# Performance work log

Hardware: AMD Instinct MI355X
Metric: run time of the kernel (lower is better)

The kernel has to match this reference:

```python
import jax, jax.numpy as jnp
import numpy as np

NX = 96
N_NODES = 6 * NX * NX          # 55296 cubed-sphere grid points
N_EDGES = 4 * N_NODES          # ~4-neighbor connectivity
HID = 32
NUM_STEPS = 3


def setup_inputs() -> dict:
    key = jax.random.key(0)
    ks = jax.random.split(key, 12)
    s = 0.05
    inp = {
        "in_node_features": jax.random.normal(ks[0], (2, 6, NX, NX, 32), jnp.float32),
        "edge_relation": jax.random.normal(ks[1], (N_EDGES, 4), jnp.float32),
        "pw1": jax.random.normal(ks[2], (32, HID), jnp.float32) * s,
        "pb1": jnp.zeros((HID,), jnp.float32),
        "pw2": jax.random.normal(ks[3], (HID, HID), jnp.float32) * s,
        "pb2": jnp.zeros((HID,), jnp.float32),
        "ew1": jax.random.normal(ks[4], (4, 32), jnp.float32) * s,
        "eb1": jnp.zeros((32,), jnp.float32),
        "ew2": jax.random.normal(ks[5], (32, HID * HID), jnp.float32) * s,
        "eb2": jnp.zeros((HID * HID,), jnp.float32),
        "conv_b": jnp.zeros((HID,), jnp.float32),
        "gru_w_ih": jax.random.normal(ks[6], (3 * HID, HID), jnp.float32) * s,
        "gru_w_hh": jax.random.normal(ks[7], (3 * HID, HID), jnp.float32) * s,
        "gru_b_ih": jnp.zeros((3 * HID,), jnp.float32),
        "gru_b_hh": jnp.zeros((3 * HID,), jnp.float32),
        "edge_src": jax.random.randint(ks[8], (N_EDGES,), 0, N_NODES, jnp.int32),
        "edge_dst": jax.random.randint(ks[9], (N_EDGES,), 0, N_NODES, jnp.int32),
    }
    return inp


def reference(in_node_features, edge_relation, pw1, pb1, pw2, pb2,
              ew1, eb1, ew2, eb2, conv_b,
              gru_w_ih, gru_w_hh, gru_b_ih, gru_b_hh,
              edge_src, edge_dst):
    B, T, nx1, nx2, C = in_node_features.shape
    N = T * nx1 * nx2
    H = pw2.shape[1]

    x = in_node_features.reshape(B, N, C)
    # project_node_features: Linear -> ReLU -> Linear
    h0 = jnp.maximum(x @ pw1 + pb1, 0.0) @ pw2 + pb2          # [B, N, H]

    # edge network (same every step): Linear -> ReLU -> Linear -> [E, H, H]
    We = (jnp.maximum(edge_relation @ ew1 + eb1, 0.0) @ ew2 + eb2)
    We = We.reshape(-1, H, H)                                  # [E, H, H]

    def seg_sum(m):  # m: [E, H] -> [N, H]
        return jax.ops.segment_sum(m, edge_dst, num_segments=N)

    def step(carry, _):
        node, hidden = carry                                   # each [B, N, H]
        # NNConv: gather src feats, per-edge matmul, scatter-sum to dst
        msg = jnp.einsum('beh,eho->beo', node[:, edge_src], We)  # [B, E, H]
        agg = jax.vmap(seg_sum)(msg) + conv_b                    # [B, N, H]
        node = jnp.maximum(agg, 0.0)                             # ReLU
        # single GRU step (seq_len = 1)
        gx = node @ gru_w_ih.T + gru_b_ih                        # [B, N, 3H]
        gh = hidden @ gru_w_hh.T + gru_b_hh
        r = jax.nn.sigmoid(gx[..., :H] + gh[..., :H])
        z = jax.nn.sigmoid(gx[..., H:2 * H] + gh[..., H:2 * H])
        n = jnp.tanh(gx[..., 2 * H:] + r * gh[..., 2 * H:])
        hidden = (1.0 - z) * n + z * hidden
        return (hidden, hidden), None

    (node, _), _ = jax.lax.scan(step, (h0, h0), None, length=NUM_STEPS)
    return node.reshape(B, T, nx1, nx2, H)
```

## Files before the change

kernel.cpp:

```cpp
#include <hip/hip_runtime.h>

typedef unsigned short u16;
typedef short s16x8 __attribute__((ext_vector_type(8)));
typedef float f32x4 __attribute__((ext_vector_type(4)));
typedef float f32x2 __attribute__((ext_vector_type(2)));

#define NNODES 55296
#define NEDGES 221184
#define ROWS   110592

__device__ __forceinline__ u16 f2bf(float f) {
    union { float f; unsigned u; } v; v.f = f;
    unsigned r = (v.u + 0x7fffu + ((v.u >> 16) & 1u)) >> 16;
    return (u16)r;
}
__device__ __forceinline__ float bf2f(u16 u) {
    return __uint_as_float(((unsigned)u) << 16);
}

__global__ __launch_bounds__(256) void pack_bfrag(
    const float* __restrict__ src, u16* __restrict__ dst_hi, u16* __restrict__ dst_lo,
    int ntiles, int ncols, int trans)
{
    int idx = blockIdx.x * 256 + threadIdx.x;
    if (idx >= ntiles * 512) return;
    int t = idx >> 9, rr = idx & 511, lane = rr >> 3, j = rr & 7;
    int k = (lane >> 4) * 8 + j;
    int n = t * 16 + (lane & 15);
    float v = trans ? src[n * 32 + k] : src[k * ncols + n];
    u16 hb = f2bf(v);
    dst_hi[idx] = hb;
    if (dst_lo) dst_lo[idx] = f2bf(v - bf2f(hb));
}

__global__ __launch_bounds__(256) void edgemlp_kernel(
    const float* __restrict__ er, const float* __restrict__ ew1,
    const float* __restrict__ eb1, u16* __restrict__ rbf)
{
    __shared__ float er_lds[32];
    __shared__ float w_lds[128];
    __shared__ float b_lds[32];
    int tid = threadIdx.x;
    int e8 = blockIdx.x * 8;
    if (tid < 32) er_lds[tid] = er[e8 * 4 + tid];
    else if (tid < 160) w_lds[tid - 32] = ew1[tid - 32];
    else if (tid < 192) b_lds[tid - 160] = eb1[tid - 160];
    __syncthreads();
    int el = tid >> 5, o = tid & 31;
    const float* e4 = er_lds + el * 4;
    float v = b_lds[o] + e4[0] * w_lds[o] + e4[1] * w_lds[32 + o]
                       + e4[2] * w_lds[64 + o] + e4[3] * w_lds[96 + o];
    rbf[(e8 + el) * 32 + o] = f2bf(fmaxf(v, 0.f));
}

__global__ __launch_bounds__(256) void nodeproj_kernel(
    const float* __restrict__ x,
    const u16* __restrict__ pw1h, const u16* __restrict__ pw1l, const float* __restrict__ pb1,
    const u16* __restrict__ pw2h, const u16* __restrict__ pw2l, const float* __restrict__ pb2,
    float* __restrict__ st_f32, u16* __restrict__ st_hi, u16* __restrict__ st_lo)
{
    __shared__ alignas(16) u16 t_hi[4][512];
    __shared__ alignas(16) u16 t_lo[4][512];
    int tid = threadIdx.x, wave = tid >> 6, lane = tid & 63;
    int quad = lane >> 4, col = lane & 15;
    int row0 = (blockIdx.x * 4 + wave) * 16;

    const float* xp = x + (row0 + col) * 32 + quad * 8;
    f32x4 xv0 = *(const f32x4*)(xp), xv1 = *(const f32x4*)(xp + 4);
    s16x8 ah, al;
#pragma unroll
    for (int i = 0; i < 4; ++i) {
        u16 h0 = f2bf(xv0[i]); ah[i] = (short)h0; al[i] = (short)f2bf(xv0[i] - bf2f(h0));
        u16 h1 = f2bf(xv1[i]); ah[4+i] = (short)h1; al[4+i] = (short)f2bf(xv1[i] - bf2f(h1));
    }
#pragma unroll
    for (int t = 0; t < 2; ++t) {
        s16x8 bh = *(const s16x8*)(pw1h + t * 512 + lane * 8);
        s16x8 bl = *(const s16x8*)(pw1l + t * 512 + lane * 8);
        f32x4 acc = {0,0,0,0};
        acc = __builtin_amdgcn_mfma_f32_16x16x32_bf16(al, bh, acc, 0,0,0);
        acc = __builtin_amdgcn_mfma_f32_16x16x32_bf16(ah, bl, acc, 0,0,0);
        acc = __builtin_amdgcn_mfma_f32_16x16x32_bf16(ah, bh, acc, 0,0,0);
        float bias = pb1[t * 16 + col];
#pragma unroll
        for (int r = 0; r < 4; ++r) {
            float v = fmaxf(acc[r] + bias, 0.f);
            u16 hb = f2bf(v);
            int idx = (quad * 4 + r) * 32 + t * 16 + col;
            t_hi[wave][idx] = hb;
            t_lo[wave][idx] = f2bf(v - bf2f(hb));
        }
    }
    __syncthreads();
    s16x8 th = *(const s16x8*)(&t_hi[wave][col * 32 + quad * 8]);
    s16x8 tl = *(const s16x8*)(&t_lo[wave][col * 32 + quad * 8]);
#pragma unroll
    for (int t = 0; t < 2; ++t) {
        s16x8 bh = *(const s16x8*)(pw2h + t * 512 + lane * 8);
        s16x8 bl = *(const s16x8*)(pw2l + t * 512 + lane * 8);
        f32x4 acc = {0,0,0,0};
        acc = __builtin_amdgcn_mfma_f32_16x16x32_bf16(tl, bh, acc, 0,0,0);
        acc = __builtin_amdgcn_mfma_f32_16x16x32_bf16(th, bl, acc, 0,0,0);
        acc = __builtin_amdgcn_mfma_f32_16x16x32_bf16(th, bh, acc, 0,0,0);
        float bias = pb2[t * 16 + col];
#pragma unroll
        for (int r = 0; r < 4; ++r) {
            float v = acc[r] + bias;
            int row = row0 + quad * 4 + r;
            int o = t * 16 + col;
            st_f32[row * 32 + o] = v;
            u16 hb = f2bf(v);
            st_hi[row * 32 + o] = hb;
            st_lo[row * 32 + o] = f2bf(v - bf2f(hb));
        }
    }
}

__global__ __launch_bounds__(256) void msg_kernel(
    const u16* __restrict__ rbf, const u16* __restrict__ ew2f,
    const float* __restrict__ eb2, const float* __restrict__ state,
    const int* __restrict__ esrc, const int* __restrict__ edst,
    float* __restrict__ agg)
{
    __shared__ alignas(16) float eb2_lds[1024];
    __shared__ alignas(16) float ns_lds[4][16 * 68];
    int tid = threadIdx.x;
    {
        *(f32x4*)(eb2_lds + tid * 4) = *(const f32x4*)(eb2 + tid * 4);
    }
    int wave = tid >> 6, lane = tid & 63;
    int quad = lane >> 4, col = lane & 15;
    int e0 = (blockIdx.x * 4 + wave) * 16;

    s16x8 afrag = *(const s16x8*)(rbf + (e0 + col) * 32 + quad * 8);

    {
        int el = lane >> 2, part = lane & 3;
        int b = part >> 1, half = part & 1;
        int src = esrc[e0 + el];
        const float* sp = state + (b * NNODES + src) * 32 + half * 16;
        float* dp = &ns_lds[wave][el * 68 + b * 32 + half * 16];
        *(f32x4*)(dp + 0)  = *(const f32x4*)(sp + 0);
        *(f32x4*)(dp + 4)  = *(const f32x4*)(sp + 4);
        *(f32x4*)(dp + 8)  = *(const f32x4*)(sp + 8);
        *(f32x4*)(dp + 12) = *(const f32x4*)(sp + 12);
    }
    int dstid[4];
#pragma unroll
    for (int r = 0; r < 4; ++r) dstid[r] = edst[e0 + quad * 4 + r];
    __syncthreads();

    float msg[2][2][4] = {};
    const float* nsw = &ns_lds[wave][0];
#pragma unroll 4
    for (int hh = 0; hh < 16; ++hh) {
        int h0 = hh * 2, h1 = hh * 2 + 1;
        s16x8 b0 = *(const s16x8*)(ew2f + (4 * hh + 0) * 512 + lane * 8);
        s16x8 b1 = *(const s16x8*)(ew2f + (4 * hh + 1) * 512 + lane * 8);
        s16x8 b2 = *(const s16x8*)(ew2f + (4 * hh + 2) * 512 + lane * 8);
        s16x8 b3 = *(const s16x8*)(ew2f + (4 * hh + 3) * 512 + lane * 8);
        f32x4 z = {0,0,0,0};
        f32x4 d0 = __builtin_amdgcn_mfma_f32_16x16x32_bf16(afrag, b0, z, 0,0,0);
        f32x4 d1 = __builtin_amdgcn_mfma_f32_16x16x32_bf16(afrag, b1, z, 0,0,0);
        f32x4 d2 = __builtin_amdgcn_mfma_f32_16x16x32_bf16(afrag, b2, z, 0,0,0);
        f32x4 d3 = __builtin_amdgcn_mfma_f32_16x16x32_bf16(afrag, b3, z, 0,0,0);
        float e00 = eb2_lds[h0 * 32 + col],      e01 = eb2_lds[h0 * 32 + 16 + col];
        float e10 = eb2_lds[h1 * 32 + col],      e11 = eb2_lds[h1 * 32 + 16 + col];
#pragma unroll
        for (int r = 0; r < 4; ++r) {
            int e = quad * 4 + r;
            f32x2 n0 = *(const f32x2*)(nsw + e * 68 + 0 * 32 + h0);
            f32x2 n1 = *(const f32x2*)(nsw + e * 68 + 1 * 32 + h0);
            float w00 = d0[r] + e00, w01 = d1[r] + e01;
            float w10 = d2[r] + e10, w11 = d3[r] + e11;
            msg[0][0][r] += n0.x * w00 + n0.y * w10;
            msg[0][1][r] += n0.x * w01 + n0.y * w11;
            msg[1][0][r] += n1.x * w00 + n1.y * w10;
            msg[1][1][r] += n1.x * w01 + n1.y * w11;
        }
    }
#pragma unroll
    for (int r = 0; r < 4; ++r) {
#pragma unroll
        for (int b = 0; b < 2; ++b) {
            float* base = agg + (b * NNODES + dstid[r]) * 32;
            unsafeAtomicAdd(base + col,      msg[b][0][r]);
            unsafeAtomicAdd(base + 16 + col, msg[b][1][r]);
        }
    }
}

__global__ __launch_bounds__(256) void gru_kernel(
    const float* __restrict__ agg, const float* __restrict__ conv_b,
    const float* __restrict__ st_f32, const u16* __restrict__ st_hi, const u16* __restrict__ st_lo,
    const u16* __restrict__ wihh, const u16* __restrict__ wihl,
    const u16* __restrict__ whhh, const u16* __restrict__ whhl,
    const float* __restrict__ b_ih, const float* __restrict__ b_hh,
    float* __restrict__ out_f32, u16* __restrict__ out_hi, u16* __restrict__ out_lo)
{
    int tid = threadIdx.x, wave = tid >> 6, lane = tid & 63;
    int quad = lane >> 4, col = lane & 15;
    int row0 = (blockIdx.x * 4 + wave) * 16;

    const float* ap = agg + (row0 + col) * 32 + quad * 8;
    f32x4 av0 = *(const f32x4*)(ap), av1 = *(const f32x4*)(ap + 4);
    const float* cb = conv_b + quad * 8;
    f32x4 cb0 = *(const f32x4*)(cb), cb1 = *(const f32x4*)(cb + 4);
    s16x8 anh, anl;
#pragma unroll
    for (int i = 0; i < 4; ++i) {
        float v0 = fmaxf(av0[i] + cb0[i], 0.f);
        float v1 = fmaxf(av1[i] + cb1[i], 0.f);
        u16 h0 = f2bf(v0); anh[i] = (short)h0;   anl[i] = (short)f2bf(v0 - bf2f(h0));
        u16 h1 = f2bf(v1); anh[4+i] = (short)h1; anl[4+i] = (short)f2bf(v1 - bf2f(h1));
    }
    s16x8 ahh = *(const s16x8*)(st_hi + (row0 + col) * 32 + quad * 8);
    s16x8 ahl = *(const s16x8*)(st_lo + (row0 + col) * 32 + quad * 8);

    f32x4 gx[6], gh[6];
#pragma unroll
    for (int t = 0; t < 6; ++t) {
        s16x8 bh = *(const s16x8*)(wihh + t * 512 + lane * 8);
        s16x8 bl = *(const s16x8*)(wihl + t * 512 + lane * 8);
        f32x4 acc = {0,0,0,0};
        acc = __builtin_amdgcn_mfma_f32_16x16x32_bf16(anl, bh, acc, 0,0,0);
        acc = __builtin_amdgcn_mfma_f32_16x16x32_bf16(anh, bl, acc, 0,0,0);
        acc = __builtin_amdgcn_mfma_f32_16x16x32_bf16(anh, bh, acc, 0,0,0);
        gx[t] = acc;
        s16x8 ch = *(const s16x8*)(whhh + t * 512 + lane * 8);
        s16x8 cl = *(const s16x8*)(whhl + t * 512 + lane * 8);
        f32x4 acc2 = {0,0,0,0};
        acc2 = __builtin_amdgcn_mfma_f32_16x16x32_bf16(ahl, ch, acc2, 0,0,0);
        acc2 = __builtin_amdgcn_mfma_f32_16x16x32_bf16(ahh, cl, acc2, 0,0,0);
        acc2 = __builtin_amdgcn_mfma_f32_16x16x32_bf16(ahh, ch, acc2, 0,0,0);
        gh[t] = acc2;
    }
    float bihv[6], bhhv[6];
#pragma unroll
    for (int t = 0; t < 6; ++t) { bihv[t] = b_ih[t * 16 + col]; bhhv[t] = b_hh[t * 16 + col]; }

#pragma unroll
    for (int r = 0; r < 4; ++r) {
        int row = row0 + quad * 4 + r;
#pragma unroll
        for (int oh = 0; oh < 2; ++oh) {
            int o = oh * 16 + col;
            float hid = st_f32[row * 32 + o];
            float sr = (gx[oh][r] + bihv[oh]) + (gh[oh][r] + bhhv[oh]);
            float sz = (gx[2+oh][r] + bihv[2+oh]) + (gh[2+oh][r] + bhhv[2+oh]);
            float gxn = gx[4+oh][r] + bihv[4+oh];
            float ghn = gh[4+oh][r] + bhhv[4+oh];
            float rr = 1.f / (1.f + __expf(-sr));
            float zz = 1.f / (1.f + __expf(-sz));
            float narg = gxn + rr * ghn;
            float ex = __expf(2.f * narg);
            float nn = (ex - 1.f) / (ex + 1.f);
            float hnew = (1.f - zz) * nn + zz * hid;
            out_f32[row * 32 + o] = hnew;
            u16 hb = f2bf(hnew);
            out_hi[row * 32 + o] = hb;
            out_lo[row * 32 + o] = f2bf(hnew - bf2f(hb));
        }
    }
}

extern "C" void kernel_launch(void* const* d_in, const int* in_sizes, int n_in,
                              void* d_out, int out_size, void* d_ws, size_t ws_size,
                              hipStream_t stream)
{
    const float* x      = (const float*)d_in[0];
    const float* er     = (const float*)d_in[1];
    const float* pw1    = (const float*)d_in[2];
    const float* pb1    = (const float*)d_in[3];
    const float* pw2    = (const float*)d_in[4];
    const float* pb2    = (const float*)d_in[5];
    const float* ew1    = (const float*)d_in[6];
    const float* eb1    = (const float*)d_in[7];
    const float* ew2    = (const float*)d_in[8];
    const float* eb2    = (const float*)d_in[9];
    const float* conv_b = (const float*)d_in[10];
    const float* wih    = (const float*)d_in[11];
    const float* whh    = (const float*)d_in[12];
    const float* bih    = (const float*)d_in[13];
    const float* bhh    = (const float*)d_in[14];
    const int*   esrc   = (const int*)d_in[15];
    const int*   edst   = (const int*)d_in[16];
    float* out = (float*)d_out;

    char* ws = (char*)d_ws;
    size_t off = 0;
    auto alloc = [&](size_t bytes) -> void* {
        void* p = ws + off;
        off = (off + bytes + 255) & ~(size_t)255;
        return p;
    };
    u16*   rbf    = (u16*)  alloc((size_t)NEDGES * 32 * 2);
    float* st_f32 = (float*)alloc((size_t)ROWS * 32 * 4);
    u16*   st_hi  = (u16*)  alloc((size_t)ROWS * 32 * 2);
    u16*   st_lo  = (u16*)  alloc((size_t)ROWS * 32 * 2);
    float* agg    = (float*)alloc((size_t)ROWS * 32 * 4);
    u16*   ew2f   = (u16*)  alloc(64 * 512 * 2);
    u16*   pw1h   = (u16*)  alloc(2 * 512 * 2);
    u16*   pw1l   = (u16*)  alloc(2 * 512 * 2);
    u16*   pw2h   = (u16*)  alloc(2 * 512 * 2);
    u16*   pw2l   = (u16*)  alloc(2 * 512 * 2);
    u16*   wihhf  = (u16*)  alloc(6 * 512 * 2);
    u16*   wihlf  = (u16*)  alloc(6 * 512 * 2);
    u16*   whhhf  = (u16*)  alloc(6 * 512 * 2);
    u16*   whhlf  = (u16*)  alloc(6 * 512 * 2);
    (void)in_sizes; (void)n_in; (void)out_size; (void)ws_size;

    pack_bfrag<<<128, 256, 0, stream>>>(ew2, ew2f, (u16*)nullptr, 64, 1024, 0);
    pack_bfrag<<<4,   256, 0, stream>>>(pw1, pw1h, pw1l, 2, 32, 0);
    pack_bfrag<<<4,   256, 0, stream>>>(pw2, pw2h, pw2l, 2, 32, 0);
    pack_bfrag<<<12,  256, 0, stream>>>(wih, wihhf, wihlf, 6, 96, 1);
    pack_bfrag<<<12,  256, 0, stream>>>(whh, whhhf, whhlf, 6, 96, 1);

    edgemlp_kernel<<<NEDGES / 8, 256, 0, stream>>>(er, ew1, eb1, rbf);
    nodeproj_kernel<<<ROWS / 64, 256, 0, stream>>>(x, pw1h, pw1l, pb1, pw2h, pw2l, pb2,
                                                   st_f32, st_hi, st_lo);
    for (int s = 0; s < 3; ++s) {
        hipMemsetAsync(agg, 0, (size_t)ROWS * 32 * 4, stream);
        msg_kernel<<<NEDGES / 64, 256, 0, stream>>>(rbf, ew2f, eb2, st_f32, esrc, edst, agg);
        float* of = (s == 2) ? out : st_f32;
        gru_kernel<<<ROWS / 64, 256, 0, stream>>>(agg, conv_b, st_f32, st_hi, st_lo,
                                                  wihhf, wihlf, whhhf, whhlf, bih, bhh,
                                                  of, st_hi, st_lo);
    }
}
```

Baseline: 388.2 us.

## Sort edges by destination into CSR and aggregate messages in LDS

Builds a CSR ordering of edges by destination using a histogram, a three-stage scan and a scatter, then permutes the edge-MLP output to match. The message kernel becomes destination-node-centric: each wave handles 16 destination nodes, walks their edge range in chunks of 16, accumulates into LDS with shared atomics, and writes agg directly. This removes the per-step memset and the global float atomics. In exchange it adds several preprocessing launches, load imbalance from variable degree, and partially filled MFMA tiles wasted at chunk boundaries.

```diff
diff --git a/kernel.cpp b/kernel.cpp
--- a/kernel.cpp
+++ b/kernel.cpp
@@ -8,6 +8,7 @@
 #define NNODES 55296
 #define NEDGES 221184
 #define ROWS   110592
+#define NBLK_SCAN 216
 
 __device__ __forceinline__ u16 f2bf(float f) {
     union { float f; unsigned u; } v; v.f = f;
@@ -16,6 +17,69 @@
 }
 __device__ __forceinline__ float bf2f(u16 u) {
     return __uint_as_float(((unsigned)u) << 16);
+}
+
+__global__ __launch_bounds__(256) void hist_kernel(
+    const int* __restrict__ edst, int* __restrict__ cnt)
+{
+    int i = blockIdx.x * 256 + threadIdx.x;
+    atomicAdd(&cnt[edst[i]], 1);
+}
+
+__global__ __launch_bounds__(256) void scan1_kernel(
+    const int* __restrict__ cnt, int* __restrict__ exc, int* __restrict__ bsum)
+{
+    __shared__ int s[256];
+    int t = threadIdx.x, g = blockIdx.x * 256 + t;
+    int v = cnt[g];
+    s[t] = v; __syncthreads();
+#pragma unroll
+    for (int d = 1; d < 256; d <<= 1) {
+        int x = (t >= d) ? s[t - d] : 0;
+        __syncthreads();
+        s[t] += x;
+        __syncthreads();
+    }
+    exc[g] = s[t] - v;
+    if (t == 255) bsum[blockIdx.x] = s[255];
+}
+
+__global__ __launch_bounds__(256) void scan2_kernel(
+    const int* __restrict__ bsum, int* __restrict__ bofs)
+{
+    __shared__ int s[256];
+    int t = threadIdx.x;
+    int v = (t < NBLK_SCAN) ? bsum[t] : 0;
+    s[t] = v; __syncthreads();
+#pragma unroll
+    for (int d = 1; d < 256; d <<= 1) {
+        int x = (t >= d) ? s[t - d] : 0;
+        __syncthreads();
+        s[t] += x;
+        __syncthreads();
+    }
+    if (t < NBLK_SCAN) bofs[t] = s[t] - v;
+}
+
+__global__ __launch_bounds__(256) void scan3_kernel(
+    const int* __restrict__ exc, const int* __restrict__ bofs, int* __restrict__ rowstart)
+{
+    int g = blockIdx.x * 256 + threadIdx.x;
+    rowstart[g] = exc[g] + bofs[blockIdx.x];
+    if (g == 0) rowstart[NNODES] = NEDGES;
+}
+
+__global__ __launch_bounds__(256) void scatter_kernel(
+    const int* __restrict__ edst, const int* __restrict__ esrc,
+    const int* __restrict__ rowstart, int* __restrict__ cursor,
+    int* __restrict__ perm, int* __restrict__ esrcp, int* __restrict__ edstp)
+{
+    int i = blockIdx.x * 256 + threadIdx.x;
+    int d = edst[i];
+    int pos = rowstart[d] + atomicAdd(&cursor[d], 1);
+    perm[pos] = i;
+    esrcp[pos] = esrc[i];
+    edstp[pos] = d;
 }
 
 __global__ __launch_bounds__(256) void pack_bfrag(
@@ -35,14 +99,18 @@
 
 __global__ __launch_bounds__(256) void edgemlp_kernel(
     const float* __restrict__ er, const float* __restrict__ ew1,
-    const float* __restrict__ eb1, u16* __restrict__ rbf)
+    const float* __restrict__ eb1, const int* __restrict__ perm,
+    u16* __restrict__ rbf)
 {
     __shared__ float er_lds[32];
     __shared__ float w_lds[128];
     __shared__ float b_lds[32];
     int tid = threadIdx.x;
     int e8 = blockIdx.x * 8;
-    if (tid < 32) er_lds[tid] = er[e8 * 4 + tid];
+    if (tid < 32) {
+        int e = perm[e8 + (tid >> 2)];
+        er_lds[tid] = er[e * 4 + (tid & 3)];
+    }
     else if (tid < 160) w_lds[tid - 32] = ew1[tid - 32];
     else if (tid < 192) b_lds[tid - 160] = eb1[tid - 160];
     __syncthreads();
@@ -119,74 +187,98 @@
 __global__ __launch_bounds__(256) void msg_kernel(
     const u16* __restrict__ rbf, const u16* __restrict__ ew2f,
     const float* __restrict__ eb2, const float* __restrict__ state,
-    const int* __restrict__ esrc, const int* __restrict__ edst,
+    const int* __restrict__ esrcp, const int* __restrict__ edstp,
+    const int* __restrict__ rowstart,
     float* __restrict__ agg)
 {
     __shared__ alignas(16) float eb2_lds[1024];
     __shared__ alignas(16) float ns_lds[4][16 * 68];
+    __shared__ alignas(16) float agg_lds[4][16 * 68];
     int tid = threadIdx.x;
     {
         *(f32x4*)(eb2_lds + tid * 4) = *(const f32x4*)(eb2 + tid * 4);
     }
     int wave = tid >> 6, lane = tid & 63;
     int quad = lane >> 4, col = lane & 15;
-    int e0 = (blockIdx.x * 4 + wave) * 16;
-
-    s16x8 afrag = *(const s16x8*)(rbf + (e0 + col) * 32 + quad * 8);
-
-    {
-        int el = lane >> 2, part = lane & 3;
-        int b = part >> 1, half = part & 1;
-        int src = esrc[e0 + el];
-        const float* sp = state + (b * NNODES + src) * 32 + half * 16;
-        float* dp = &ns_lds[wave][el * 68 + b * 32 + half * 16];
-        *(f32x4*)(dp + 0)  = *(const f32x4*)(sp + 0);
-        *(f32x4*)(dp + 4)  = *(const f32x4*)(sp + 4);
-        *(f32x4*)(dp + 8)  = *(const f32x4*)(sp + 8);
-        *(f32x4*)(dp + 12) = *(const f32x4*)(sp + 12);
-    }
-    int dstid[4];
-#pragma unroll
-    for (int r = 0; r < 4; ++r) dstid[r] = edst[e0 + quad * 4 + r];
+    int n0 = (blockIdx.x * 4 + wave) * 16;
+    int base = rowstart[n0], end = rowstart[n0 + 16];
+
+    float* ag = &agg_lds[wave][0];
+    for (int i = lane; i < 16 * 68; i += 64) ag[i] = 0.f;
     __syncthreads();
 
-    float msg[2][2][4] = {};
     const float* nsw = &ns_lds[wave][0];
+    for (int p0 = base; p0 < end; p0 += 16) {
+        {
+            int el = lane >> 2, part = lane & 3;
+            int b = part >> 1, half = part & 1;
+            int p = p0 + el;
+            float* dp = &ns_lds[wave][el * 68 + b * 32 + half * 16];
+            if (p < end) {
+                int src = esrcp[p];
+                const float* sp = state + (size_t)(b * NNODES + src) * 32 + half * 16;
+                *(f32x4*)(dp + 0)  = *(const f32x4*)(sp + 0);
+                *(f32x4*)(dp + 4)  = *(const f32x4*)(sp + 4);
+                *(f32x4*)(dp + 8)  = *(const f32x4*)(sp + 8);
+                *(f32x4*)(dp + 12) = *(const f32x4*)(sp + 12);
+            } else {
+                f32x4 z = {0,0,0,0};
+                *(f32x4*)(dp + 0) = z; *(f32x4*)(dp + 4) = z;
+                *(f32x4*)(dp + 8) = z; *(f32x4*)(dp + 12) = z;
+            }
+        }
+        int dl[4];
+#pragma unroll
+        for (int r = 0; r < 4; ++r) {
+            int pr = p0 + quad * 4 + r;
+            int d = edstp[pr] - n0;
+            dl[r] = d < 0 ? 0 : (d > 15 ? 15 : d);
+        }
+        s16x8 afrag = *(const s16x8*)(rbf + (size_t)(p0 + col) * 32 + quad * 8);
+
+        float msg[2][2][4] = {};
 #pragma unroll 4
-    for (int hh = 0; hh < 16; ++hh) {
-        int h0 = hh * 2, h1 = hh * 2 + 1;
-        s16x8 b0 = *(const s16x8*)(ew2f + (4 * hh + 0) * 512 + lane * 8);
-        s16x8 b1 = *(const s16x8*)(ew2f + (4 * hh + 1) * 512 + lane * 8);
-        s16x8 b2 = *(const s16x8*)(ew2f + (4 * hh + 2) * 512 + lane * 8);
-        s16x8 b3 = *(const s16x8*)(ew2f + (4 * hh + 3) * 512 + lane * 8);
-        f32x4 z = {0,0,0,0};
-        f32x4 d0 = __builtin_amdgcn_mfma_f32_16x16x32_bf16(afrag, b0, z, 0,0,0);
-        f32x4 d1 = __builtin_amdgcn_mfma_f32_16x16x32_bf16(afrag, b1, z, 0,0,0);
-        f32x4 d2 = __builtin_amdgcn_mfma_f32_16x16x32_bf16(afrag, b2, z, 0,0,0);
-        f32x4 d3 = __builtin_amdgcn_mfma_f32_16x16x32_bf16(afrag, b3, z, 0,0,0);
-        float e00 = eb2_lds[h0 * 32 + col],      e01 = eb2_lds[h0 * 32 + 16 + col];
-        float e10 = eb2_lds[h1 * 32 + col],      e11 = eb2_lds[h1 * 32 + 16 + col];
+        for (int hh = 0; hh < 16; ++hh) {
+            int h0 = hh * 2, h1 = hh * 2 + 1;
+            s16x8 b0 = *(const s16x8*)(ew2f + (4 * hh + 0) * 512 + lane * 8);
+            s16x8 b1 = *(const s16x8*)(ew2f + (4 * hh + 1) * 512 + lane * 8);
+            s16x8 b2 = *(const s16x8*)(ew2f + (4 * hh + 2) * 512 + lane * 8);
+            s16x8 b3 = *(const s16x8*)(ew2f + (4 * hh + 3) * 512 + lane * 8);
+            f32x4 z = {0,0,0,0};
+            f32x4 d0 = __builtin_amdgcn_mfma_f32_16x16x32_bf16(afrag, b0, z, 0,0,0);
+            f32x4 d1 = __builtin_amdgcn_mfma_f32_16x16x32_bf16(afrag, b1, z, 0,0,0);
+            f32x4 d2 = __builtin_amdgcn_mfma_f32_16x16x32_bf16(afrag, b2, z, 0,0,0);
+            f32x4 d3 = __builtin_amdgcn_mfma_f32_16x16x32_bf16(afrag, b3, z, 0,0,0);
+            float e00 = eb2_lds[h0 * 32 + col],      e01 = eb2_lds[h0 * 32 + 16 + col];
+            float e10 = eb2_lds[h1 * 32 + col],      e11 = eb2_lds[h1 * 32 + 16 + col];
+#pragma unroll
+            for (int r = 0; r < 4; ++r) {
+                int e = quad * 4 + r;
+                f32x2 n0v = *(const f32x2*)(nsw + e * 68 + 0 * 32 + h0);
+                f32x2 n1v = *(const f32x2*)(nsw + e * 68 + 1 * 32 + h0);
+                float w00 = d0[r] + e00, w01 = d1[r] + e01;
+                float w10 = d2[r] + e10, w11 = d3[r] + e11;
+                msg[0][0][r] += n0v.x * w00 + n0v.y * w10;
+                msg[0][1][r] += n0v.x * w01 + n0v.y * w11;
+                msg[1][0][r] += n1v.x * w00 + n1v.y * w10;
+                msg[1][1][r] += n1v.x * w01 + n1v.y * w11;
+            }
+        }
 #pragma unroll
         for (int r = 0; r < 4; ++r) {
-            int e = quad * 4 + r;
-            f32x2 n0 = *(const f32x2*)(nsw + e * 68 + 0 * 32 + h0);
-            f32x2 n1 = *(const f32x2*)(nsw + e * 68 + 1 * 32 + h0);
-            float w00 = d0[r] + e00, w01 = d1[r] + e01;
-            float w10 = d2[r] + e10, w11 = d3[r] + e11;
-            msg[0][0][r] += n0.x * w00 + n0.y * w10;
-            msg[0][1][r] += n0.x * w01 + n0.y * w11;
-            msg[1][0][r] += n1.x * w00 + n1.y * w10;
-            msg[1][1][r] += n1.x * w01 + n1.y * w11;
-        }
-    }
-#pragma unroll
-    for (int r = 0; r < 4; ++r) {
-#pragma unroll
-        for (int b = 0; b < 2; ++b) {
-            float* base = agg + (b * NNODES + dstid[r]) * 32;
-            unsafeAtomicAdd(base + col,      msg[b][0][r]);
-            unsafeAtomicAdd(base + 16 + col, msg[b][1][r]);
-        }
+            float* abase = ag + dl[r] * 68;
+            atomicAdd(abase + col,           msg[0][0][r]);
+            atomicAdd(abase + 16 + col,      msg[0][1][r]);
+            atomicAdd(abase + 32 + col,      msg[1][0][r]);
+            atomicAdd(abase + 48 + col,      msg[1][1][r]);
+        }
+    }
+    __syncthreads();
+    for (int i = lane; i < 256; i += 64) {
+        int node = i >> 4, q = i & 15;
+        f32x4 v = *(f32x4*)(ag + node * 68 + q * 4);
+        int b = q >> 3, o = (q & 7) * 4;
+        *(f32x4*)(agg + ((size_t)(b * NNODES) + n0 + node) * 32 + o) = v;
     }
 }
 
@@ -294,7 +386,7 @@
         off = (off + bytes + 255) & ~(size_t)255;
         return p;
     };
-    u16*   rbf    = (u16*)  alloc((size_t)NEDGES * 32 * 2);
+    u16*   rbf    = (u16*)  alloc((size_t)(NEDGES + 16) * 32 * 2);
     float* st_f32 = (float*)alloc((size_t)ROWS * 32 * 4);
     u16*   st_hi  = (u16*)  alloc((size_t)ROWS * 32 * 2);
     u16*   st_lo  = (u16*)  alloc((size_t)ROWS * 32 * 2);
@@ -308,7 +400,26 @@
     u16*   wihlf  = (u16*)  alloc(6 * 512 * 2);
     u16*   whhhf  = (u16*)  alloc(6 * 512 * 2);
     u16*   whhlf  = (u16*)  alloc(6 * 512 * 2);
+    int*   cnt      = (int*)alloc((size_t)NNODES * 4);
+    int*   cursor   = (int*)alloc((size_t)NNODES * 4);
+    int*   exc      = (int*)alloc((size_t)NNODES * 4);
+    int*   bsum     = (int*)alloc(NBLK_SCAN * 4);
+    int*   bofs     = (int*)alloc(NBLK_SCAN * 4);
+    int*   rowstart = (int*)alloc((size_t)(NNODES + 1) * 4);
+    int*   perm     = (int*)alloc((size_t)NEDGES * 4);
+    int*   esrcp    = (int*)alloc((size_t)(NEDGES + 16) * 4);
+    int*   edstp    = (int*)alloc((size_t)(NEDGES + 16) * 4);
     (void)in_sizes; (void)n_in; (void)out_size; (void)ws_size;
+
+    hipMemsetAsync(cnt, 0, (size_t)NNODES * 4, stream);
+    hipMemsetAsync(cursor, 0, (size_t)NNODES * 4, stream);
+    hipMemsetAsync(rbf + (size_t)NEDGES * 32, 0, 16 * 32 * 2, stream);
+    hist_kernel<<<NEDGES / 256, 256, 0, stream>>>(edst, cnt);
+    scan1_kernel<<<NBLK_SCAN, 256, 0, stream>>>(cnt, exc, bsum);
+    scan2_kernel<<<1, 256, 0, stream>>>(bsum, bofs);
+    scan3_kernel<<<NBLK_SCAN, 256, 0, stream>>>(exc, bofs, rowstart);
+    scatter_kernel<<<NEDGES / 256, 256, 0, stream>>>(edst, esrc, rowstart, cursor,
+                                                     perm, esrcp, edstp);
 
     pack_bfrag<<<128, 256, 0, stream>>>(ew2, ew2f, (u16*)nullptr, 64, 1024, 0);
     pack_bfrag<<<4,   256, 0, stream>>>(pw1, pw1h, pw1l, 2, 32, 0);
@@ -316,12 +427,12 @@
     pack_bfrag<<<12,  256, 0, stream>>>(wih, wihhf, wihlf, 6, 96, 1);
     pack_bfrag<<<12,  256, 0, stream>>>(whh, whhhf, whhlf, 6, 96, 1);
 
-    edgemlp_kernel<<<NEDGES / 8, 256, 0, stream>>>(er, ew1, eb1, rbf);
+    edgemlp_kernel<<<NEDGES / 8, 256, 0, stream>>>(er, ew1, eb1, perm, rbf);
     nodeproj_kernel<<<ROWS / 64, 256, 0, stream>>>(x, pw1h, pw1l, pb1, pw2h, pw2l, pb2,
                                                    st_f32, st_hi, st_lo);
     for (int s = 0; s < 3; ++s) {
-        hipMemsetAsync(agg, 0, (size_t)ROWS * 32 * 4, stream);
-        msg_kernel<<<NEDGES / 64, 256, 0, stream>>>(rbf, ew2f, eb2, st_f32, esrc, edst, agg);
+        msg_kernel<<<NNODES / 64, 256, 0, stream>>>(rbf, ew2f, eb2, st_f32,
+                                                    esrcp, edstp, rowstart, agg);
         float* of = (s == 2) ? out : st_f32;
         gru_kernel<<<ROWS / 64, 256, 0, stream>>>(agg, conv_b, st_f32, st_hi, st_lo,
                                                   wihhf, wihlf, whhhf, whhlf, bih, bhh,
```

New measurement: 677.3 us. 74.5% more time.
